# Optimization experiments

Hardware: AMD Instinct MI355X
Metric: run time of the kernel (lower is better)

## Reference

```python
import jax, jax.numpy as jnp
import numpy as np

N, F, B = 16384, 1024, 512


def setup_inputs() -> dict:
    key = jax.random.key(0)
    k1, k2, k3, k4, k5 = jax.random.split(key, 5)
    s = 1.0 / np.sqrt(F + B)
    return {
        "behavior": jax.random.normal(k1, (N, B), dtype=jnp.float32),
        "h_prev": jax.random.normal(k2, (N, F), dtype=jnp.float32),
        "c_prev": jax.random.normal(k3, (N, F), dtype=jnp.float32),
        "Wh": jax.random.normal(k4, (4 * F, F), dtype=jnp.float32) * s,
        "Wx": jax.random.normal(k5, (4 * F, B), dtype=jnp.float32) * s,
        "b": jnp.zeros((4 * F,), dtype=jnp.float32),
    }


def reference(behavior, h_prev, c_prev, Wh, Wx, b):
    # Fused single GEMM for all 4 gates: [n, 4F]
    gates = jnp.einsum("nf,gf->ng", h_prev, Wh) + jnp.einsum("nb,gb->ng", behavior, Wx) + b
    i, f, g, o = jnp.split(gates, 4, axis=-1)
    i = jax.nn.sigmoid(i)
    f = jax.nn.sigmoid(f)
    g = jnp.tanh(g)
    o = jax.nn.sigmoid(o)
    c = f * c_prev + i * g
    h = o * jnp.tanh(c)
    return h
```

## Files before the change

### kernel.cpp

```cpp
#include <hip/hip_runtime.h>
#include <hip/hip_bf16.h>
#include <stdint.h>
#include <type_traits>

#define N_ROWS 16384
#define F_DIM  1024
#define B_DIM  512
#define K_DIM  1536
#define G_DIM  4096
#define NT     24
#define CB_STR 68

typedef __bf16 v8bf __attribute__((ext_vector_type(8)));
typedef float  v4f  __attribute__((ext_vector_type(4)));

typedef const void __attribute__((address_space(1)))* gptr1;
typedef void       __attribute__((address_space(3)))* lptr3;

__device__ __forceinline__ unsigned short f2bf(float x) {
    union { float f; unsigned int u; } c; c.f = x;
    unsigned int u = c.u;
    return (unsigned short)((u + 0x7FFFu + ((u >> 16) & 1u)) >> 16);
}

__device__ __forceinline__ float sigmoidf_fast(float x) {
    return 1.f / (1.f + __expf(-x));
}
__device__ __forceinline__ float tanhf_fast(float x) {
    return 1.f - 2.f / (__expf(2.f * x) + 1.f);
}

__global__ void pack_all(const float* __restrict__ behavior,
                         const float* __restrict__ h_prev,
                         const float* __restrict__ Wh,
                         const float* __restrict__ Wx,
                         const float* __restrict__ b,
                         unsigned short* __restrict__ A,
                         unsigned short* __restrict__ W,
                         float* __restrict__ bperm) {
    const int blk = blockIdx.x;
    const int col = threadIdx.x * 8;
    const float* src;
    unsigned short* dst;
    if (blk < N_ROWS) {
        src = (col < F_DIM) ? h_prev + (long)blk * F_DIM + col
                            : behavior + (long)blk * B_DIM + (col - F_DIM);
        dst = A + (long)blk * K_DIM + col;
    } else {
        const int gp   = blk - N_ROWS;
        const int gate = gp & 3;
        const int f    = gp >> 2;
        const int g    = gate * F_DIM + f;
        src = (col < F_DIM) ? Wh + (long)g * F_DIM + col
                            : Wx + (long)g * B_DIM + (col - F_DIM);
        dst = W + (long)gp * K_DIM + col;
        if (threadIdx.x == 0) bperm[gp] = b[g];
    }
    float4 lo = *(const float4*)src;
    float4 hi = *(const float4*)(src + 4);
    union { unsigned short u[8]; int4 v; } p;
    p.u[0] = f2bf(lo.x); p.u[1] = f2bf(lo.y); p.u[2] = f2bf(lo.z); p.u[3] = f2bf(lo.w);
    p.u[4] = f2bf(hi.x); p.u[5] = f2bf(hi.y); p.u[6] = f2bf(hi.z); p.u[7] = f2bf(hi.w);
    *(int4*)dst = p.v;
}

__global__ __launch_bounds__(512, 2) void lstm_gemm(
    const unsigned short* __restrict__ A,
    const unsigned short* __restrict__ W,
    const float* __restrict__ bperm,
    const float* __restrict__ c_prev,
    float* __restrict__ out)
{
    extern __shared__ char smem[];

    const int bid = blockIdx.x;
    const int s   = (bid & 7) * 128 + (bid >> 3);
    const int m0  = (s & 63) << 8;
    const int n0  = (s >> 6) << 8;

    const int tid  = threadIdx.x;
    const int lane = tid & 63;
    const int wave = tid >> 6;
    const int wmi  = wave >> 2;
    const int wni  = wave & 3;
    const int lrow = lane & 15;
    const int quad = lane >> 4;

    const int afrag = wmi * 8192 + (lane << 4);
    const int bfrag = wni * 4096 + (lane << 4);

    const unsigned short* aS0 = A + (long)(m0 + wave * 16 + lrow) * K_DIM + quad * 8;
    const unsigned short* aS1 = aS0 + (long)128 * K_DIM;
    const unsigned short* wS0 = W + (long)(n0 + wave * 16 + lrow) * K_DIM + quad * 8;
    const unsigned short* wS1 = wS0 + (long)128 * K_DIM;
    const int du0 = wave * 1024;
    const int du1 = du0 + 8192;

    v4f acc[8][4] = {};

    auto stageA = [&](int plane, int koff) {
        __builtin_amdgcn_global_load_lds((gptr1)(aS0 + koff),
                                         (lptr3)(smem + (plane << 14) + du0), 16, 0, 0);
        __builtin_amdgcn_global_load_lds((gptr1)(aS1 + koff),
                                         (lptr3)(smem + (plane << 14) + du1), 16, 0, 0);
    };
    auto stageB = [&](int plane, int koff) {
        __builtin_amdgcn_global_load_lds((gptr1)(wS0 + koff),
                                         (lptr3)(smem + 65536 + (plane << 14) + du0), 16, 0, 0);
        __builtin_amdgcn_global_load_lds((gptr1)(wS1 + koff),
                                         (lptr3)(smem + 65536 + (plane << 14) + du1), 16, 0, 0);
    };

#define MFMA_BLK(MB)                                                            \
    __builtin_amdgcn_s_setprio(1);                                              \
    _Pragma("unroll")                                                           \
    for (int mt = 0; mt < 4; ++mt)                                              \
        _Pragma("unroll")                                                       \
        for (int nt = 0; nt < 4; ++nt)                                          \
            acc[(MB)*4 + mt][nt] = __builtin_amdgcn_mfma_f32_16x16x32_bf16(     \
                afr[mt], bfr[nt], acc[(MB)*4 + mt][nt], 0, 0, 0);               \
    __builtin_amdgcn_s_setprio(0);

    auto tile = [&](int BUF, int kn, auto pf_tag) {
        constexpr bool PF = decltype(pf_tag)::value;
        const char* A0p = smem + ((BUF * 2 + 0) << 14);
        const char* A1p = smem + ((BUF * 2 + 1) << 14);
        const char* B0p = A0p + 65536;
        const char* B1p = A1p + 65536;
        const int   pb  = (BUF ^ 1) * 2;
        v8bf afr[4], bfr[4];

#pragma unroll
        for (int nt = 0; nt < 4; ++nt) bfr[nt] = *(const v8bf*)(B0p + bfrag + nt * 1024);
#pragma unroll
        for (int mt = 0; mt < 4; ++mt) afr[mt] = *(const v8bf*)(A0p + afrag + mt * 1024);
        if constexpr (PF) stageA(pb + 0, kn);
        __builtin_amdgcn_s_barrier();
        asm volatile("s_waitcnt lgkmcnt(0)" ::: "memory");
        MFMA_BLK(0)
        __builtin_amdgcn_s_barrier();

#pragma unroll
        for (int mt = 0; mt < 4; ++mt) afr[mt] = *(const v8bf*)(A0p + afrag + (4 + mt) * 1024);
        if constexpr (PF) {
            stageB(pb + 0, kn);
            asm volatile("s_waitcnt vmcnt(4)" ::: "memory");
        } else {
            asm volatile("s_waitcnt vmcnt(0)" ::: "memory");
        }
        __builtin_amdgcn_s_barrier();
        asm volatile("s_waitcnt lgkmcnt(0)" ::: "memory");
        MFMA_BLK(1)
        __builtin_amdgcn_s_barrier();

#pragma unroll
        for (int nt = 0; nt < 4; ++nt) bfr[nt] = *(const v8bf*)(B1p + bfrag + nt * 1024);
#pragma unroll
        for (int mt = 0; mt < 4; ++mt) afr[mt] = *(const v8bf*)(A1p + afrag + mt * 1024);
        if constexpr (PF) stageA(pb + 1, kn + 32);
        __builtin_amdgcn_s_barrier();
        asm volatile("s_waitcnt lgkmcnt(0)" ::: "memory");
        MFMA_BLK(0)
        __builtin_amdgcn_s_barrier();

#pragma unroll
        for (int mt = 0; mt < 4; ++mt) afr[mt] = *(const v8bf*)(A1p + afrag + (4 + mt) * 1024);
        if constexpr (PF) {
            stageB(pb + 1, kn + 32);
            asm volatile("s_waitcnt vmcnt(4)" ::: "memory");
        }
        __builtin_amdgcn_s_barrier();
        asm volatile("s_waitcnt lgkmcnt(0)" ::: "memory");
        MFMA_BLK(1)
        __builtin_amdgcn_s_barrier();
    };

    stageA(0, 0);  stageB(0, 0);
    stageA(1, 32); stageB(1, 32);
    asm volatile("s_waitcnt vmcnt(4)" ::: "memory");
    __builtin_amdgcn_s_barrier();

    int kn = 64;
    for (int t = 0; t < NT - 1; ++t) {
        tile(t & 1, kn, std::true_type{});
        kn += 64;
    }
    tile((NT - 1) & 1, 0, std::false_type{});
#undef MFMA_BLK

    float* cbuf = (float*)smem;
    const int fbase = n0 >> 2;
#pragma unroll
    for (int i = 0; i < 8; ++i) {
        const int q  = i * 512 + tid;
        const int r  = q >> 4;
        const int c4 = (q & 15) << 2;
        *(float4*)&cbuf[r * CB_STR + c4] =
            *(const float4*)&c_prev[(long)(m0 + r) * F_DIM + fbase + c4];
    }
    __syncthreads();

    const int l3 = lane & 3;
    const int fl = (lane >> 2) & 3;
#pragma unroll
    for (int nt = 0; nt < 4; ++nt) {
        const int   gcol = n0 + wni * 64 + nt * 16 + lrow;
        const float bias = bperm[gcol];
#pragma unroll
        for (int mt = 0; mt < 8; ++mt) {
            float a0 = acc[mt][nt][0] + bias;
            float a1 = acc[mt][nt][1] + bias;
            float a2 = acc[mt][nt][2] + bias;
            float a3 = acc[mt][nt][3] + bias;
            float s0 = (lane & 1) ? a0 : a1;
            float s1 = (lane & 1) ? a2 : a3;
            float t0 = __shfl_xor(s0, 1, 64);
            float t1 = __shfl_xor(s1, 1, 64);
            if (lane & 1) { a0 = t0; a2 = t1; } else { a1 = t0; a3 = t1; }
            s0 = (lane & 2) ? a0 : a2;
            s1 = (lane & 2) ? a1 : a3;
            t0 = __shfl_xor(s0, 2, 64);
            t1 = __shfl_xor(s1, 2, 64);
            if (lane & 2) { a0 = t0; a1 = t1; } else { a2 = t0; a3 = t1; }
            const float iv = sigmoidf_fast(a0);
            const float fv = sigmoidf_fast(a1);
            const float gv = tanhf_fast(a2);
            const float ov = sigmoidf_fast(a3);
            const int lr = wmi * 128 + mt * 16 + quad * 4 + l3;
            const int lc = wni * 16 + nt * 4 + fl;
            const float cp = cbuf[lr * CB_STR + lc];
            const float cv = fv * cp + iv * gv;
            cbuf[lr * CB_STR + lc] = ov * tanhf_fast(cv);
        }
    }
    __syncthreads();

#pragma unroll
    for (int i = 0; i < 8; ++i) {
        const int q  = i * 512 + tid;
        const int r  = q >> 4;
        const int c4 = (q & 15) << 2;
        *(float4*)&out[(long)(m0 + r) * F_DIM + fbase + c4] =
            *(const float4*)&cbuf[r * CB_STR + c4];
    }
}

extern "C" void kernel_launch(void* const* d_in, const int* in_sizes, int n_in,
                              void* d_out, int out_size, void* d_ws, size_t ws_size,
                              hipStream_t stream) {
    const float* behavior = (const float*)d_in[0];
    const float* h_prev   = (const float*)d_in[1];
    const float* c_prev   = (const float*)d_in[2];
    const float* Wh       = (const float*)d_in[3];
    const float* Wx       = (const float*)d_in[4];
    const float* b        = (const float*)d_in[5];
    float* out = (float*)d_out;

    unsigned short* A  = (unsigned short*)d_ws;
    unsigned short* W  = A + (size_t)N_ROWS * K_DIM;
    float*       bperm = (float*)(W + (size_t)G_DIM * K_DIM);

    hipFuncSetAttribute(reinterpret_cast<const void*>(lstm_gemm),
                        hipFuncAttributeMaxDynamicSharedMemorySize, 131072);

    pack_all<<<N_ROWS + G_DIM, 192, 0, stream>>>(behavior, h_prev, Wh, Wx, b, A, W, bperm);
    lstm_gemm<<<dim3((N_ROWS / 256) * (G_DIM / 256)), 512, 131072, stream>>>(A, W, bperm, c_prev, out);
}
```

Measured before the change: 446.0 us.

## Stage full 64-wide K tiles into XOR-swizzled LDS and drop block remap

Replaces the two 32-wide K half-planes per buffer with a single 64-wide K tile per buffer, written with an XOR chunk swizzle so fragment reads avoid LDS bank conflicts. Each wave now issues four 16-byte global-to-LDS loads per operand per tile, and prefetches wait fully on vmcnt(0) at the end of each tile instead of overlapping partially. The grouped block-to-tile mapping is replaced with a plain row-major mapping (n fastest), which changes L2 reuse of A and W tiles across concurrently running blocks.

```diff
diff --git a/kernel.cpp b/kernel.cpp
--- a/kernel.cpp
+++ b/kernel.cpp
@@ -74,9 +74,8 @@
     extern __shared__ char smem[];
 
     const int bid = blockIdx.x;
-    const int s   = (bid & 7) * 128 + (bid >> 3);
-    const int m0  = (s & 63) << 8;
-    const int n0  = (s >> 6) << 8;
+    const int n0  = (bid & 15) << 8;
+    const int m0  = (bid >> 4) << 8;
 
     const int tid  = threadIdx.x;
     const int lane = tid & 63;
@@ -86,29 +85,26 @@
     const int lrow = lane & 15;
     const int quad = lane >> 4;
 
-    const int afrag = wmi * 8192 + (lane << 4);
-    const int bfrag = wni * 4096 + (lane << 4);
-
-    const unsigned short* aS0 = A + (long)(m0 + wave * 16 + lrow) * K_DIM + quad * 8;
-    const unsigned short* aS1 = aS0 + (long)128 * K_DIM;
-    const unsigned short* wS0 = W + (long)(n0 + wave * 16 + lrow) * K_DIM + quad * 8;
-    const unsigned short* wS1 = wS0 + (long)128 * K_DIM;
-    const int du0 = wave * 1024;
-    const int du1 = du0 + 8192;
+    const int g7  = lrow & 7;
+    const int cs0 = (quad ^ g7) << 4;
+    const int cs1 = ((4 + quad) ^ g7) << 4;
+    const int aRd = wmi * 16384 + lrow * 128;
+    const int bRd = wni * 8192  + lrow * 128;
+
+    const int srow = lane >> 3;
+    const int schk = (lane & 7) ^ srow;
+    const unsigned short* sA = A + (long)(m0 + wave * 8 + srow) * K_DIM + schk * 8;
+    const unsigned short* sB = W + (long)(n0 + wave * 8 + srow) * K_DIM + schk * 8;
+    const int sDst = wave * 1024;
 
     v4f acc[8][4] = {};
 
-    auto stageA = [&](int plane, int koff) {
-        __builtin_amdgcn_global_load_lds((gptr1)(aS0 + koff),
-                                         (lptr3)(smem + (plane << 14) + du0), 16, 0, 0);
-        __builtin_amdgcn_global_load_lds((gptr1)(aS1 + koff),
-                                         (lptr3)(smem + (plane << 14) + du1), 16, 0, 0);
-    };
-    auto stageB = [&](int plane, int koff) {
-        __builtin_amdgcn_global_load_lds((gptr1)(wS0 + koff),
-                                         (lptr3)(smem + 65536 + (plane << 14) + du0), 16, 0, 0);
-        __builtin_amdgcn_global_load_lds((gptr1)(wS1 + koff),
-                                         (lptr3)(smem + 65536 + (plane << 14) + du1), 16, 0, 0);
+    auto stage4 = [&](const unsigned short* src, int ldsbase, int koff) {
+#pragma unroll
+        for (int u = 0; u < 4; ++u)
+            __builtin_amdgcn_global_load_lds(
+                (gptr1)(src + (long)u * 64 * K_DIM + koff),
+                (lptr3)(smem + ldsbase + u * 8192 + sDst), 16, 0, 0);
     };
 
 #define MFMA_BLK(MB)                                                            \
@@ -123,61 +119,50 @@
 
     auto tile = [&](int BUF, int kn, auto pf_tag) {
         constexpr bool PF = decltype(pf_tag)::value;
-        const char* A0p = smem + ((BUF * 2 + 0) << 14);
-        const char* A1p = smem + ((BUF * 2 + 1) << 14);
-        const char* B0p = A0p + 65536;
-        const char* B1p = A1p + 65536;
-        const int   pb  = (BUF ^ 1) * 2;
+        const int Ab = BUF * 32768;
+        const int Bb = 65536 + Ab;
+        const int Pb = (BUF ^ 1) * 32768;
         v8bf afr[4], bfr[4];
 
 #pragma unroll
-        for (int nt = 0; nt < 4; ++nt) bfr[nt] = *(const v8bf*)(B0p + bfrag + nt * 1024);
-#pragma unroll
-        for (int mt = 0; mt < 4; ++mt) afr[mt] = *(const v8bf*)(A0p + afrag + mt * 1024);
-        if constexpr (PF) stageA(pb + 0, kn);
+        for (int nt = 0; nt < 4; ++nt) bfr[nt] = *(const v8bf*)(smem + Bb + bRd + nt * 2048 + cs0);
+#pragma unroll
+        for (int mt = 0; mt < 4; ++mt) afr[mt] = *(const v8bf*)(smem + Ab + aRd + mt * 2048 + cs0);
+        if constexpr (PF) stage4(sA, Pb, kn);
         __builtin_amdgcn_s_barrier();
         asm volatile("s_waitcnt lgkmcnt(0)" ::: "memory");
         MFMA_BLK(0)
         __builtin_amdgcn_s_barrier();
 
 #pragma unroll
-        for (int mt = 0; mt < 4; ++mt) afr[mt] = *(const v8bf*)(A0p + afrag + (4 + mt) * 1024);
-        if constexpr (PF) {
-            stageB(pb + 0, kn);
-            asm volatile("s_waitcnt vmcnt(4)" ::: "memory");
-        } else {
-            asm volatile("s_waitcnt vmcnt(0)" ::: "memory");
-        }
+        for (int mt = 0; mt < 4; ++mt) afr[mt] = *(const v8bf*)(smem + Ab + aRd + (4 + mt) * 2048 + cs0);
+        if constexpr (PF) stage4(sB, 65536 + Pb, kn);
         __builtin_amdgcn_s_barrier();
         asm volatile("s_waitcnt lgkmcnt(0)" ::: "memory");
         MFMA_BLK(1)
         __builtin_amdgcn_s_barrier();
 
 #pragma unroll
-        for (int nt = 0; nt < 4; ++nt) bfr[nt] = *(const v8bf*)(B1p + bfrag + nt * 1024);
-#pragma unroll
-        for (int mt = 0; mt < 4; ++mt) afr[mt] = *(const v8bf*)(A1p + afrag + mt * 1024);
-        if constexpr (PF) stageA(pb + 1, kn + 32);
+        for (int nt = 0; nt < 4; ++nt) bfr[nt] = *(const v8bf*)(smem + Bb + bRd + nt * 2048 + cs1);
+#pragma unroll
+        for (int mt = 0; mt < 4; ++mt) afr[mt] = *(const v8bf*)(smem + Ab + aRd + mt * 2048 + cs1);
         __builtin_amdgcn_s_barrier();
         asm volatile("s_waitcnt lgkmcnt(0)" ::: "memory");
         MFMA_BLK(0)
         __builtin_amdgcn_s_barrier();
 
 #pragma unroll
-        for (int mt = 0; mt < 4; ++mt) afr[mt] = *(const v8bf*)(A1p + afrag + (4 + mt) * 1024);
-        if constexpr (PF) {
-            stageB(pb + 1, kn + 32);
-            asm volatile("s_waitcnt vmcnt(4)" ::: "memory");
-        }
+        for (int mt = 0; mt < 4; ++mt) afr[mt] = *(const v8bf*)(smem + Ab + aRd + (4 + mt) * 2048 + cs1);
+        asm volatile("s_waitcnt vmcnt(0)" ::: "memory");
         __builtin_amdgcn_s_barrier();
         asm volatile("s_waitcnt lgkmcnt(0)" ::: "memory");
         MFMA_BLK(1)
         __builtin_amdgcn_s_barrier();
     };
 
-    stageA(0, 0);  stageB(0, 0);
-    stageA(1, 32); stageB(1, 32);
-    asm volatile("s_waitcnt vmcnt(4)" ::: "memory");
+    stage4(sA, 0, 0);
+    stage4(sB, 65536, 0);
+    asm volatile("s_waitcnt vmcnt(0)" ::: "memory");
     __builtin_amdgcn_s_barrier();
 
     int kn = 64;
```

Measured after the change: 418.8 us. 6.1% less time.
